# Performance work log

Hardware: AMD Instinct MI355X
Metric: run time of the kernel (lower is better)

Reference implementation:

```python
import jax, jax.numpy as jnp
import numpy as np

D_OUT = 8192
D_IN = 8192
BA = 64  # block size for A (output side)
BB = 64  # block size for B (input side)
NA = D_OUT // BA
NB = D_IN // BB


def setup_inputs() -> dict:
    key = jax.random.key(0)
    k1, k2, k3 = jax.random.split(key, 3)
    # W plays the role of naive_compression_module.reconstruct(): dense d_out x d_in
    W = jax.random.normal(k1, (D_OUT, D_IN), dtype=jnp.float32)
    # Block-diagonal A (d_out x d_out) stored as stack of diagonal blocks [nA, bA, bA]
    A_blocks = jax.random.normal(k2, (NA, BA, BA), dtype=jnp.float32)
    # Block-diagonal B (d_in x d_in) stored as [nB, bB, bB]
    B_blocks = jax.random.normal(k3, (NB, BB, BB), dtype=jnp.float32)
    return {"W": W, "A_blocks": A_blocks, "B_blocks": B_blocks}


def reference(W, A_blocks, B_blocks):
    # out = A @ W @ B with A, B block-diagonal; skip the zero off-diagonal blocks.
    nA, bA, _ = A_blocks.shape
    nB, bB, _ = B_blocks.shape
    d_out = nA * bA
    d_in = nB * bB
    # Left multiply: each A block acts on its own bA-row slab of W.
    # [nA, bA, bA] @ [nA, bA, d_in] -> [nA, bA, d_in]
    AW = jnp.einsum('nab,nbj->naj', A_blocks, W.reshape(nA, bA, d_in)).reshape(d_out, d_in)
    # Right multiply: each B block acts on its own bB-column slab.
    # [d_out, nB, bB] @ [nB, bB, bB] -> [d_out, nB, bB]
    out = jnp.einsum('inb,nbc->inc', AW.reshape(d_out, nB, bB), B_blocks).reshape(d_out, d_in)
    return out
```

## Files before the change

### kernel.cpp

```cpp
#include <hip/hip_runtime.h>


#define D 8192
#define BS 64
#define LSTR 72

typedef __bf16 bf16x8 __attribute__((ext_vector_type(8)));
typedef float  f32x4  __attribute__((ext_vector_type(4)));

__device__ __forceinline__ unsigned short f2bf(float f) {
    union { float f; unsigned u; } v; v.f = f;
    unsigned r = v.u + 0x7FFFu + ((v.u >> 16) & 1u);
    return (unsigned short)(r >> 16);
}

__global__ __launch_bounds__(256, 4) void bcl_kernel(
    const float* __restrict__ W,
    const float* __restrict__ Ab,
    const float* __restrict__ Bb,
    float* __restrict__ out)
{
    __shared__ __align__(16) unsigned short Wl[BS * LSTR];
    __shared__ __align__(16) unsigned short Al[BS * LSTR];
    __shared__ __align__(16) unsigned short Bt[BS * LSTR];
    __shared__ __align__(16) unsigned short Tt[BS * LSTR];

    const int t = threadIdx.x;
    const int b = blockIdx.x;
    const int a = blockIdx.y;

    const float* Wg = W  + (size_t)a * BS * D + (size_t)b * BS;
    const float* Ag = Ab + (size_t)a * BS * BS;
    const float* Bg = Bb + (size_t)b * BS * BS;

    #pragma unroll
    for (int i = 0; i < 4; ++i) {
        int lin = i * 256 + t;
        int row = lin >> 4;
        int c4  = (lin & 15) << 2;
        f32x4 w  = *(const f32x4*)(Wg + (size_t)row * D + c4);
        f32x4 av = *(const f32x4*)(Ag + row * BS + c4);
        f32x4 bv = *(const f32x4*)(Bg + row * BS + c4);
        uint2 wp, ap;
        wp.x = (unsigned)f2bf(w[0])  | ((unsigned)f2bf(w[1])  << 16);
        wp.y = (unsigned)f2bf(w[2])  | ((unsigned)f2bf(w[3])  << 16);
        ap.x = (unsigned)f2bf(av[0]) | ((unsigned)f2bf(av[1]) << 16);
        ap.y = (unsigned)f2bf(av[2]) | ((unsigned)f2bf(av[3]) << 16);
        *(uint2*)&Wl[row * LSTR + c4] = wp;
        *(uint2*)&Al[row * LSTR + c4] = ap;
        Bt[(c4 + 0) * LSTR + row] = f2bf(bv[0]);
        Bt[(c4 + 1) * LSTR + row] = f2bf(bv[1]);
        Bt[(c4 + 2) * LSTR + row] = f2bf(bv[2]);
        Bt[(c4 + 3) * LSTR + row] = f2bf(bv[3]);
    }
    __syncthreads();

    const int lane = t & 63;
    const int wv   = t >> 6;
    const int l16  = lane & 15;
    const int quad = lane >> 4;
    const int m0   = wv * 16;

    f32x4 acc[4] = {};
    #pragma unroll
    for (int s = 0; s < 2; ++s) {
        const int k0 = s * 32 + quad * 8;
        bf16x8 af = *(const bf16x8*)&Wl[(m0 + l16) * LSTR + k0];
        #pragma unroll
        for (int j = 0; j < 4; ++j) {
            bf16x8 bf = *(const bf16x8*)&Bt[(j * 16 + l16) * LSTR + k0];
            acc[j] = __builtin_amdgcn_mfma_f32_16x16x32_bf16(af, bf, acc[j], 0, 0, 0);
        }
    }

    #pragma unroll
    for (int j = 0; j < 4; ++j) {
        uint2 p;
        p.x = (unsigned)f2bf(acc[j][0]) | ((unsigned)f2bf(acc[j][1]) << 16);
        p.y = (unsigned)f2bf(acc[j][2]) | ((unsigned)f2bf(acc[j][3]) << 16);
        *(uint2*)&Tt[(j * 16 + l16) * LSTR + m0 + quad * 4] = p;
    }
    __syncthreads();

    f32x4 acc2[4] = {};
    #pragma unroll
    for (int s = 0; s < 2; ++s) {
        const int k0 = s * 32 + quad * 8;
        bf16x8 af = *(const bf16x8*)&Al[(m0 + l16) * LSTR + k0];
        #pragma unroll
        for (int j = 0; j < 4; ++j) {
            bf16x8 bf = *(const bf16x8*)&Tt[(j * 16 + l16) * LSTR + k0];
            acc2[j] = __builtin_amdgcn_mfma_f32_16x16x32_bf16(af, bf, acc2[j], 0, 0, 0);
        }
    }

    float* Og = out + (size_t)a * BS * D + (size_t)b * BS;
    #pragma unroll
    for (int j = 0; j < 4; ++j) {
        #pragma unroll
        for (int r = 0; r < 4; ++r) {
            Og[(size_t)(m0 + quad * 4 + r) * D + j * 16 + l16] = acc2[j][r];
        }
    }
}

extern "C" void kernel_launch(void* const* d_in, const int* in_sizes, int n_in,
                              void* d_out, int out_size, void* d_ws, size_t ws_size,
                              hipStream_t stream) {
    const float* W = (const float*)d_in[0];
    const float* A = (const float*)d_in[1];
    const float* B = (const float*)d_in[2];
    float* o = (float*)d_out;
    dim3 grid(D / BS, D / BS);
    bcl_kernel<<<grid, 256, 0, stream>>>(W, A, B, o);
}
```

Before: 453.7 us.

## Stage output through LDS for vectorized nontemporal stores and batch global loads

The epilogue now writes results to a padded LDS tile and then emits 16-byte nontemporal global stores, replacing the scalar strided stores. All global loads are issued up front, with W loaded nontemporally. A's LDS conversion is deferred until after the first MFMA phase, and bf16 packing uses the hardware paired conversion intrinsic. This adds two barriers and reuses the W region of LDS for the output tile, which the new barrier protects.

Result: faster. 434.9 us (-4.2%).

```diff
diff --git a/kernel.cpp b/kernel.cpp
--- a/kernel.cpp
+++ b/kernel.cpp
@@ -1,17 +1,25 @@
 #include <hip/hip_runtime.h>
+#include <hip/hip_bf16.h>
 
 
 #define D 8192
 #define BS 64
 #define LSTR 72
+#define OSTR 68
 
-typedef __bf16 bf16x8 __attribute__((ext_vector_type(8)));
-typedef float  f32x4  __attribute__((ext_vector_type(4)));
+typedef __bf16  bf16x8 __attribute__((ext_vector_type(8)));
+typedef float   f32x4  __attribute__((ext_vector_type(4)));
 
 __device__ __forceinline__ unsigned short f2bf(float f) {
     union { float f; unsigned u; } v; v.f = f;
     unsigned r = v.u + 0x7FFFu + ((v.u >> 16) & 1u);
     return (unsigned short)(r >> 16);
+}
+
+__device__ __forceinline__ unsigned pkbf(float lo, float hi) {
+    union { __hip_bfloat162 h; unsigned u; } c;
+    c.h = __float22bfloat162_rn(make_float2(lo, hi));
+    return c.u;
 }
 
 __global__ __launch_bounds__(256, 4) void bcl_kernel(
@@ -20,10 +28,12 @@
     const float* __restrict__ Bb,
     float* __restrict__ out)
 {
-    __shared__ __align__(16) unsigned short Wl[BS * LSTR];
-    __shared__ __align__(16) unsigned short Al[BS * LSTR];
-    __shared__ __align__(16) unsigned short Bt[BS * LSTR];
-    __shared__ __align__(16) unsigned short Tt[BS * LSTR];
+    __shared__ __align__(16) unsigned char smem[36864];
+    unsigned short* Wl = (unsigned short*)(smem);
+    unsigned short* Al = (unsigned short*)(smem + 9216);
+    unsigned short* Bt = (unsigned short*)(smem + 18432);
+    unsigned short* Tt = (unsigned short*)(smem + 27648);
+    float*          Ol = (float*)(smem);
 
     const int t = threadIdx.x;
     const int b = blockIdx.x;
@@ -33,25 +43,29 @@
     const float* Ag = Ab + (size_t)a * BS * BS;
     const float* Bg = Bb + (size_t)b * BS * BS;
 
+    const int r0 = t >> 4;
+    const int c4 = (t & 15) << 2;
+
+    f32x4 w[4], av[4], bv[4];
     #pragma unroll
     for (int i = 0; i < 4; ++i) {
-        int lin = i * 256 + t;
-        int row = lin >> 4;
-        int c4  = (lin & 15) << 2;
-        f32x4 w  = *(const f32x4*)(Wg + (size_t)row * D + c4);
-        f32x4 av = *(const f32x4*)(Ag + row * BS + c4);
-        f32x4 bv = *(const f32x4*)(Bg + row * BS + c4);
-        uint2 wp, ap;
-        wp.x = (unsigned)f2bf(w[0])  | ((unsigned)f2bf(w[1])  << 16);
-        wp.y = (unsigned)f2bf(w[2])  | ((unsigned)f2bf(w[3])  << 16);
-        ap.x = (unsigned)f2bf(av[0]) | ((unsigned)f2bf(av[1]) << 16);
-        ap.y = (unsigned)f2bf(av[2]) | ((unsigned)f2bf(av[3]) << 16);
+        const int row = i * 16 + r0;
+        w[i]  = __builtin_nontemporal_load((const f32x4*)(Wg + (size_t)row * D + c4));
+        av[i] = *(const f32x4*)(Ag + row * BS + c4);
+        bv[i] = *(const f32x4*)(Bg + row * BS + c4);
+    }
+
+    #pragma unroll
+    for (int i = 0; i < 4; ++i) {
+        const int row = i * 16 + r0;
+        uint2 wp;
+        wp.x = pkbf(w[i][0], w[i][1]);
+        wp.y = pkbf(w[i][2], w[i][3]);
         *(uint2*)&Wl[row * LSTR + c4] = wp;
-        *(uint2*)&Al[row * LSTR + c4] = ap;
-        Bt[(c4 + 0) * LSTR + row] = f2bf(bv[0]);
-        Bt[(c4 + 1) * LSTR + row] = f2bf(bv[1]);
-        Bt[(c4 + 2) * LSTR + row] = f2bf(bv[2]);
-        Bt[(c4 + 3) * LSTR + row] = f2bf(bv[3]);
+        Bt[(c4 + 0) * LSTR + row] = f2bf(bv[i][0]);
+        Bt[(c4 + 1) * LSTR + row] = f2bf(bv[i][1]);
+        Bt[(c4 + 2) * LSTR + row] = f2bf(bv[i][2]);
+        Bt[(c4 + 3) * LSTR + row] = f2bf(bv[i][3]);
     }
     __syncthreads();
 
@@ -74,10 +88,19 @@
     }
 
     #pragma unroll
+    for (int i = 0; i < 4; ++i) {
+        const int row = i * 16 + r0;
+        uint2 ap;
+        ap.x = pkbf(av[i][0], av[i][1]);
+        ap.y = pkbf(av[i][2], av[i][3]);
+        *(uint2*)&Al[row * LSTR + c4] = ap;
+    }
+
+    #pragma unroll
     for (int j = 0; j < 4; ++j) {
         uint2 p;
-        p.x = (unsigned)f2bf(acc[j][0]) | ((unsigned)f2bf(acc[j][1]) << 16);
-        p.y = (unsigned)f2bf(acc[j][2]) | ((unsigned)f2bf(acc[j][3]) << 16);
+        p.x = pkbf(acc[j][0], acc[j][1]);
+        p.y = pkbf(acc[j][2], acc[j][3]);
         *(uint2*)&Tt[(j * 16 + l16) * LSTR + m0 + quad * 4] = p;
     }
     __syncthreads();
@@ -93,14 +116,23 @@
             acc2[j] = __builtin_amdgcn_mfma_f32_16x16x32_bf16(af, bf, acc2[j], 0, 0, 0);
         }
     }
+    __syncthreads();
 
-    float* Og = out + (size_t)a * BS * D + (size_t)b * BS;
     #pragma unroll
     for (int j = 0; j < 4; ++j) {
         #pragma unroll
         for (int r = 0; r < 4; ++r) {
-            Og[(size_t)(m0 + quad * 4 + r) * D + j * 16 + l16] = acc2[j][r];
+            Ol[(m0 + quad * 4 + r) * OSTR + j * 16 + l16] = acc2[j][r];
         }
+    }
+    __syncthreads();
+
+    float* Og = out + (size_t)a * BS * D + (size_t)b * BS;
+    #pragma unroll
+    for (int i = 0; i < 4; ++i) {
+        const int row = i * 16 + r0;
+        f32x4 v = *(const f32x4*)&Ol[row * OSTR + c4];
+        __builtin_nontemporal_store(v, (f32x4*)(Og + (size_t)row * D + c4));
     }
 }
 
```
